# Optimization experiments

Measured on AMD Instinct MI355X. Metric: run time of the kernel, lower is better.

Reference implementation:

```python
import jax, jax.numpy as jnp
import numpy as np

N_NODES = 50000


def sage_conv(x, edge_index, W_l, b_l, W_r):
    # PyG SAGEConv (mean aggr): out_i = lin_l(mean_{j->i} x_j) + lin_r(x_i)
    src, dst = edge_index[0], edge_index[1]
    msgs = x[src]                                        # [E, C] gather
    summed = jax.ops.segment_sum(msgs, dst, num_segments=N_NODES)  # [N, C]
    deg = jax.ops.segment_sum(jnp.ones((edge_index.shape[1],), x.dtype), dst,
                              num_segments=N_NODES)
    mean = summed / jnp.maximum(deg, 1.0)[:, None]
    return mean @ W_l + b_l + x @ W_r


def setup_inputs() -> dict:
    key = jax.random.key(0)
    ks = jax.random.split(key, 12)
    E, EL, C, X = 800000, 1000000, 128, 384
    return {
        "x": jax.random.normal(ks[0], (N_NODES, X), jnp.float32),
        "edge_index": jax.random.randint(ks[1], (2, E), 0, N_NODES),
        "edge_label_index": jax.random.randint(ks[2], (2, EL), 0, N_NODES),
        "W_lin": jax.random.normal(ks[3], (X, C), jnp.float32) * 0.05,
        "b_lin": jax.random.normal(ks[4], (C,), jnp.float32) * 0.05,
        "W1_l": jax.random.normal(ks[5], (C, C), jnp.float32) * 0.08,
        "b1": jax.random.normal(ks[6], (C,), jnp.float32) * 0.05,
        "W1_r": jax.random.normal(ks[7], (C, C), jnp.float32) * 0.08,
        "W2_l": jax.random.normal(ks[8], (C, C), jnp.float32) * 0.08,
        "b2": jax.random.normal(ks[9], (C,), jnp.float32) * 0.05,
        "W2_r": jax.random.normal(ks[10], (C, C), jnp.float32) * 0.08,
    }


def reference(x, edge_index, edge_label_index, W_lin, b_lin,
              W1_l, b1, W1_r, W2_l, b2, W2_r):
    h = x @ W_lin + b_lin                                # label_lin
    h = jax.nn.relu(sage_conv(h, edge_index, W1_l, b1, W1_r))
    h = sage_conv(h, edge_index, W2_l, b2, W2_r)
    # Classifier: dot product of head/tail node features per label edge
    head = h[edge_label_index[0]]
    tail = h[edge_label_index[1]]
    return (head * tail).sum(axis=-1)                    # [EL]
```

## Files before the change

### kernel.cpp

```cpp
#include <hip/hip_runtime.h>

#define NODES 50000
#define CH 128
#define ELLW 64

using frag_ab = __attribute__((ext_vector_type(8))) short;
using frag_cd = __attribute__((ext_vector_type(4))) float;

__device__ __forceinline__ float bf2f(ushort u) {
    union { unsigned u; float f; } v; v.u = ((unsigned)u) << 16; return v.f;
}
__device__ __forceinline__ ushort f2bf(float f) {
    union { float f; unsigned u; } v; v.f = f;
    unsigned r = v.u + 0x7fff + ((v.u >> 16) & 1);
    return (ushort)(r >> 16);
}

__global__ void prep_weights(const float* __restrict__ Wlin,
                             const float* __restrict__ W1l, const float* __restrict__ W1r,
                             const float* __restrict__ W2l, const float* __restrict__ W2r,
                             ushort* __restrict__ o0, ushort* __restrict__ o1,
                             ushort* __restrict__ o2, ushort* __restrict__ o3,
                             ushort* __restrict__ o4, int* __restrict__ degs) {
    int b = blockIdx.x;
    if (b >= 448) {
        int i = (b - 448) * 256 + threadIdx.y * 128 + threadIdx.x;
        if (i < NODES) degs[i << 4] = 0;
        return;
    }
    const float* W; ushort* O; int K; int kb;
    if (b < 192) { W = Wlin; O = o0; K = 384; kb = b; }
    else {
        int j = (b - 192) >> 6; kb = (b - 192) & 63; K = 128;
        W = (j == 0) ? W1l : (j == 1) ? W1r : (j == 2) ? W2l : W2r;
        O = (j == 0) ? o1  : (j == 1) ? o2  : (j == 2) ? o3  : o4;
    }
    int k = kb * 2 + threadIdx.y;
    int n = threadIdx.x;
    if (k < K) O[(size_t)n * K + k] = f2bf(W[(size_t)k * 128 + n]);
}

__global__ __launch_bounds__(256) void lin_and_ell(
    const float* __restrict__ A, const ushort* __restrict__ Wt,
    const float* __restrict__ bias, ushort* __restrict__ out, int N, int GB,
    const int* __restrict__ ei, int E, int* __restrict__ degs, ushort* __restrict__ ell)
{
    __shared__ ushort As[128 * 32];
    __shared__ ushort Bs[128 * 32];
    if (blockIdx.x >= GB) {
        int e0 = ((blockIdx.x - GB) * 256 + threadIdx.x) * 4;
        if (e0 >= E) return;
        int s[4], dd[4], cnt;
        if (((E & 3) == 0) && (e0 + 3 < E)) {
            int4 sv = *(const int4*)(ei + e0);
            int4 dv = *(const int4*)(ei + E + e0);
            s[0] = sv.x; s[1] = sv.y; s[2] = sv.z; s[3] = sv.w;
            dd[0] = dv.x; dd[1] = dv.y; dd[2] = dv.z; dd[3] = dv.w;
            cnt = 4;
        } else {
            cnt = E - e0; if (cnt > 4) cnt = 4;
#pragma unroll
            for (int j = 0; j < 4; ++j) {
                int e = (j < cnt) ? e0 + j : e0;
                s[j] = ei[e]; dd[j] = ei[E + e];
            }
        }
#pragma unroll
        for (int j = 0; j < 4; ++j) {
            if (j < cnt) {
                int pos = atomicAdd(&degs[dd[j] << 4], 1);
                if (pos < ELLW) ell[(size_t)dd[j] * ELLW + pos] = (ushort)s[j];
            }
        }
        return;
    }
    const int tid = threadIdx.x;
    const int lane = tid & 63;
    const int wave = tid >> 6;
    const int wr = wave >> 1, wc = wave & 1;
    const int row0 = blockIdx.x * 128;
    const int l15 = lane & 15, quad = lane >> 4;

    frag_cd acc[4][4];
#pragma unroll
    for (int i = 0; i < 4; ++i)
#pragma unroll
        for (int j = 0; j < 4; ++j) acc[i][j] = (frag_cd){0.f, 0.f, 0.f, 0.f};

#pragma unroll 1
    for (int k0 = 0; k0 < 384; k0 += 32) {
        __syncthreads();
#pragma unroll
        for (int i = 0; i < 4; ++i) {
            int e = i * 256 + tid;
            int r = e >> 3, q = e & 7;
            int gr = row0 + r; if (gr > N - 1) gr = N - 1;
            float4 v = *(const float4*)(A + (size_t)gr * 384 + k0 + q * 4);
            ushort4 o; o.x = f2bf(v.x); o.y = f2bf(v.y); o.z = f2bf(v.z); o.w = f2bf(v.w);
            *(ushort4*)(As + r * 32 + q * 4) = o;
        }
#pragma unroll
        for (int i = 0; i < 2; ++i) {
            int e = i * 256 + tid;
            uint4 v = *(const uint4*)(Wt + (size_t)(e >> 2) * 384 + k0 + (e & 3) * 8);
            *(uint4*)(Bs + e * 8) = v;
        }
        __syncthreads();

        frag_ab a[4], b[4];
#pragma unroll
        for (int i = 0; i < 4; ++i)
            a[i] = *(const frag_ab*)(As + (wr * 64 + i * 16 + l15) * 32 + quad * 8);
#pragma unroll
        for (int j = 0; j < 4; ++j)
            b[j] = *(const frag_ab*)(Bs + (wc * 64 + j * 16 + l15) * 32 + quad * 8);
#pragma unroll
        for (int i = 0; i < 4; ++i)
#pragma unroll
            for (int j = 0; j < 4; ++j)
                acc[i][j] = __builtin_amdgcn_mfma_f32_16x16x32_bf16(a[i], b[j], acc[i][j], 0, 0, 0);
    }

#pragma unroll
    for (int i = 0; i < 4; ++i)
#pragma unroll
        for (int r = 0; r < 4; ++r) {
            int row = row0 + wr * 64 + i * 16 + quad * 4 + r;
            if (row < N)
#pragma unroll
                for (int j = 0; j < 4; ++j) {
                    int col = wc * 64 + j * 16 + l15;
                    out[(size_t)row * 128 + col] = f2bf(acc[i][j][r] + bias[col]);
                }
        }
}

__device__ __forceinline__ void acc8(float* acc, uint4 v) {
    acc[0] += bf2f((ushort)(v.x & 0xffff)); acc[1] += bf2f((ushort)(v.x >> 16));
    acc[2] += bf2f((ushort)(v.y & 0xffff)); acc[3] += bf2f((ushort)(v.y >> 16));
    acc[4] += bf2f((ushort)(v.z & 0xffff)); acc[5] += bf2f((ushort)(v.z >> 16));
    acc[6] += bf2f((ushort)(v.w & 0xffff)); acc[7] += bf2f((ushort)(v.w >> 16));
}

template <bool RELU>
__global__ __launch_bounds__(256) void agg_gemm(
    const ushort* __restrict__ h, const ushort* __restrict__ ell,
    const int* __restrict__ degs,
    const ushort* __restrict__ Wtl, const ushort* __restrict__ Wtr,
    const float* __restrict__ bias, ushort* __restrict__ out, int N)
{
    __shared__ ushort Ms[64 * 128];
    __shared__ ushort As[64 * 32];
    __shared__ ushort Bs[128 * 32];
    const int tid = threadIdx.x;
    const int lane = tid & 63;
    const int wave = tid >> 6;
    const int row0 = blockIdx.x * 64;
    const int g = lane >> 4;
    const int q = lane & 15;

#pragma unroll 1
    for (int it = 0; it < 4; ++it) {
        int r = (wave << 4) + (it << 2) + g;
        int node = row0 + r;
        int nd = node < N ? node : N - 1;
        const ushort* erow = ell + (size_t)nd * ELLW;
        int d = degs[nd << 4];
        int dc = d < ELLW ? d : ELLW;
        float acc[8];
#pragma unroll
        for (int k = 0; k < 8; ++k) acc[k] = 0.f;
        int n = 0;
        for (; n + 8 <= dc; n += 8) {
            ushort4 iv0 = *(const ushort4*)(erow + n);
            ushort4 iv1 = *(const ushort4*)(erow + n + 4);
            uint4 v0 = *(const uint4*)(h + (size_t)iv0.x * CH + q * 8);
            uint4 v1 = *(const uint4*)(h + (size_t)iv0.y * CH + q * 8);
            uint4 v2 = *(const uint4*)(h + (size_t)iv0.z * CH + q * 8);
            uint4 v3 = *(const uint4*)(h + (size_t)iv0.w * CH + q * 8);
            uint4 v4 = *(const uint4*)(h + (size_t)iv1.x * CH + q * 8);
            uint4 v5 = *(const uint4*)(h + (size_t)iv1.y * CH + q * 8);
            uint4 v6 = *(const uint4*)(h + (size_t)iv1.z * CH + q * 8);
            uint4 v7 = *(const uint4*)(h + (size_t)iv1.w * CH + q * 8);
            acc8(acc, v0); acc8(acc, v1); acc8(acc, v2); acc8(acc, v3);
            acc8(acc, v4); acc8(acc, v5); acc8(acc, v6); acc8(acc, v7);
        }
        for (; n + 4 <= dc; n += 4) {
            ushort4 iv = *(const ushort4*)(erow + n);
            uint4 v0 = *(const uint4*)(h + (size_t)iv.x * CH + q * 8);
            uint4 v1 = *(const uint4*)(h + (size_t)iv.y * CH + q * 8);
            uint4 v2 = *(const uint4*)(h + (size_t)iv.z * CH + q * 8);
            uint4 v3 = *(const uint4*)(h + (size_t)iv.w * CH + q * 8);
            acc8(acc, v0); acc8(acc, v1); acc8(acc, v2); acc8(acc, v3);
        }
        for (; n < dc; ++n) {
            uint4 v0 = *(const uint4*)(h + (size_t)erow[n] * CH + q * 8);
            acc8(acc, v0);
        }
        float inv = 1.f / fmaxf((float)d, 1.f);
        uint4 o;
        o.x = ((uint)f2bf(acc[1] * inv) << 16) | (uint)f2bf(acc[0] * inv);
        o.y = ((uint)f2bf(acc[3] * inv) << 16) | (uint)f2bf(acc[2] * inv);
        o.z = ((uint)f2bf(acc[5] * inv) << 16) | (uint)f2bf(acc[4] * inv);
        o.w = ((uint)f2bf(acc[7] * inv) << 16) | (uint)f2bf(acc[6] * inv);
        int chunk = q ^ (r & 7);
        *(uint4*)(Ms + r * 128 + chunk * 8) = o;
    }

    const int wr = wave >> 1, wc = wave & 1;
    const int l15 = q, quad = g;

    frag_cd acc2[2][4];
#pragma unroll
    for (int i = 0; i < 2; ++i)
#pragma unroll
        for (int j = 0; j < 4; ++j) acc2[i][j] = (frag_cd){0.f, 0.f, 0.f, 0.f};

#pragma unroll 1
    for (int part = 0; part < 2; ++part) {
        const ushort* Wt = part ? Wtr : Wtl;
#pragma unroll 1
        for (int k0 = 0; k0 < 128; k0 += 32) {
            __syncthreads();
            if (part) {
                int rr = tid >> 2, kq = tid & 3;
                int gr = row0 + rr; if (gr > N - 1) gr = N - 1;
                uint4 v = *(const uint4*)(h + (size_t)gr * CH + k0 + kq * 8);
                *(uint4*)(As + rr * 32 + ((kq ^ (rr & 3)) * 8)) = v;
            }
#pragma unroll
            for (int i2 = 0; i2 < 2; ++i2) {
                int e = i2 * 256 + tid;
                int br = e >> 2, bk = e & 3;
                uint4 v = *(const uint4*)(Wt + (size_t)br * 128 + k0 + bk * 8);
                *(uint4*)(Bs + br * 32 + ((bk ^ (br & 3)) * 8)) = v;
            }
            __syncthreads();

            frag_ab a[2], b[4];
#pragma unroll
            for (int i = 0; i < 2; ++i) {
                int ar = wr * 32 + i * 16 + l15;
                if (part) {
                    a[i] = *(const frag_ab*)(As + ar * 32 + ((quad ^ (ar & 3)) * 8));
                } else {
                    int ch = ((k0 >> 3) + quad) ^ (ar & 7);
                    a[i] = *(const frag_ab*)(Ms + ar * 128 + ch * 8);
                }
            }
#pragma unroll
            for (int j = 0; j < 4; ++j) {
                int br = wc * 64 + j * 16 + l15;
                b[j] = *(const frag_ab*)(Bs + br * 32 + ((quad ^ (br & 3)) * 8));
            }
#pragma unroll
            for (int i = 0; i < 2; ++i)
#pragma unroll
                for (int j = 0; j < 4; ++j)
                    acc2[i][j] = __builtin_amdgcn_mfma_f32_16x16x32_bf16(a[i], b[j], acc2[i][j], 0, 0, 0);
        }
    }

#pragma unroll
    for (int i = 0; i < 2; ++i)
#pragma unroll
        for (int rr = 0; rr < 4; ++rr) {
            int row = row0 + wr * 32 + i * 16 + quad * 4 + rr;
            if (row < N)
#pragma unroll
                for (int j = 0; j < 4; ++j) {
                    int col = wc * 64 + j * 16 + l15;
                    float v = acc2[i][j][rr] + bias[col];
                    if (RELU) v = fmaxf(v, 0.f);
                    out[(size_t)row * 128 + col] = f2bf(v);
                }
        }
}

__device__ __forceinline__ float dot8(uint4 va, uint4 vb) {
    float p = 0.f;
    p += bf2f((ushort)(va.x & 0xffff)) * bf2f((ushort)(vb.x & 0xffff));
    p += bf2f((ushort)(va.x >> 16))    * bf2f((ushort)(vb.x >> 16));
    p += bf2f((ushort)(va.y & 0xffff)) * bf2f((ushort)(vb.y & 0xffff));
    p += bf2f((ushort)(va.y >> 16))    * bf2f((ushort)(vb.y >> 16));
    p += bf2f((ushort)(va.z & 0xffff)) * bf2f((ushort)(vb.z & 0xffff));
    p += bf2f((ushort)(va.z >> 16))    * bf2f((ushort)(vb.z >> 16));
    p += bf2f((ushort)(va.w & 0xffff)) * bf2f((ushort)(vb.w & 0xffff));
    p += bf2f((ushort)(va.w >> 16))    * bf2f((ushort)(vb.w >> 16));
    return p;
}

__global__ __launch_bounds__(256) void classify_bf(
    const ushort* __restrict__ h2, const int* __restrict__ eli,
    int EL, float* __restrict__ out) {
    int gt = blockIdx.x * blockDim.x + threadIdx.x;
    int g0 = (gt >> 4) * 8;
    int lane = gt & 15;
    if (g0 >= EL) return;
    bool full = (g0 + 7 < EL);
    int ha[8], ta[8];
    if (full) {
        int4 h0 = *(const int4*)(eli + g0);
        int4 h1 = *(const int4*)(eli + g0 + 4);
        int4 t0 = *(const int4*)(eli + EL + g0);
        int4 t1 = *(const int4*)(eli + EL + g0 + 4);
        ha[0] = h0.x; ha[1] = h0.y; ha[2] = h0.z; ha[3] = h0.w;
        ha[4] = h1.x; ha[5] = h1.y; ha[6] = h1.z; ha[7] = h1.w;
        ta[0] = t0.x; ta[1] = t0.y; ta[2] = t0.z; ta[3] = t0.w;
        ta[4] = t1.x; ta[5] = t1.y; ta[6] = t1.z; ta[7] = t1.w;
    } else {
#pragma unroll
        for (int j = 0; j < 8; ++j) {
            int gj = (g0 + j < EL) ? g0 + j : EL - 1;
            ha[j] = eli[gj];
            ta[j] = eli[EL + gj];
        }
    }
    uint4 va[8], vb[8];
#pragma unroll
    for (int j = 0; j < 8; ++j) {
        va[j] = *((const uint4*)(h2 + (size_t)ha[j] * CH) + lane);
        vb[j] = *((const uint4*)(h2 + (size_t)ta[j] * CH) + lane);
    }
    float p[8];
#pragma unroll
    for (int j = 0; j < 8; ++j) p[j] = dot8(va[j], vb[j]);
#pragma unroll
    for (int s = 8; s >= 1; s >>= 1) {
#pragma unroll
        for (int j = 0; j < 8; ++j) p[j] += __shfl_down(p[j], s, 16);
    }
    if (lane == 0) {
        if (full) {
            *(float4*)(out + g0)     = make_float4(p[0], p[1], p[2], p[3]);
            *(float4*)(out + g0 + 4) = make_float4(p[4], p[5], p[6], p[7]);
        } else {
#pragma unroll
            for (int j = 0; j < 8; ++j)
                if (g0 + j < EL) out[g0 + j] = p[j];
        }
    }
}

extern "C" void kernel_launch(void* const* d_in, const int* in_sizes, int n_in,
                              void* d_out, int out_size, void* d_ws, size_t ws_size,
                              hipStream_t stream) {
    const float* x     = (const float*)d_in[0];
    const int*   ei    = (const int*)d_in[1];
    const int*   eli   = (const int*)d_in[2];
    const float* W_lin = (const float*)d_in[3];
    const float* b_lin = (const float*)d_in[4];
    const float* W1l   = (const float*)d_in[5];
    const float* b1    = (const float*)d_in[6];
    const float* W1r   = (const float*)d_in[7];
    const float* W2l   = (const float*)d_in[8];
    const float* b2    = (const float*)d_in[9];
    const float* W2r   = (const float*)d_in[10];
    float* out = (float*)d_out;

    const int E  = in_sizes[1] / 2;
    const int EL = in_sizes[2] / 2;
    const int N  = NODES;

    char* ws = (char*)d_ws;
    size_t off = 0;
    auto alloc = [&](size_t bytes) -> void* {
        void* p = ws + off;
        off += (bytes + 255) & ~(size_t)255;
        return p;
    };
    ushort* n0    = (ushort*)alloc((size_t)N * CH * sizeof(ushort));
    ushort* n1    = (ushort*)alloc((size_t)N * CH * sizeof(ushort));
    ushort* n2    = (ushort*)alloc((size_t)N * CH * sizeof(ushort));
    ushort* WtLin = (ushort*)alloc((size_t)CH * 384 * sizeof(ushort));
    ushort* Wt1l  = (ushort*)alloc((size_t)CH * CH * sizeof(ushort));
    ushort* Wt1r  = (ushort*)alloc((size_t)CH * CH * sizeof(ushort));
    ushort* Wt2l  = (ushort*)alloc((size_t)CH * CH * sizeof(ushort));
    ushort* Wt2r  = (ushort*)alloc((size_t)CH * CH * sizeof(ushort));
    int* degs = (int*)alloc((size_t)N * 16 * sizeof(int));
    ushort* ell = (ushort*)alloc((size_t)N * ELLW * sizeof(ushort));
    (void)ws_size; (void)n_in; (void)out_size;

    const int GB128 = (N + 127) / 128;
    const int EB4   = (E + 1023) / 1024;
    const int AB64  = (N + 63) / 64;

    prep_weights<<<dim3(644), dim3(128, 2), 0, stream>>>(
        W_lin, W1l, W1r, W2l, W2r, WtLin, Wt1l, Wt1r, Wt2l, Wt2r, degs);

    lin_and_ell<<<dim3(GB128 + EB4), dim3(256), 0, stream>>>(
        x, WtLin, b_lin, n0, N, GB128, ei, E, degs, ell);

    agg_gemm<true><<<dim3(AB64), dim3(256), 0, stream>>>(
        n0, ell, degs, Wt1l, Wt1r, b1, n2, N);

    agg_gemm<false><<<dim3(AB64), dim3(256), 0, stream>>>(
        n2, ell, degs, Wt2l, Wt2r, b2, n1, N);

    long long groups = ((long long)EL + 7) / 8;
    long long cls_threads = groups * 16;
    classify_bf<<<dim3((int)((cls_threads + 255) / 256)), dim3(256), 0, stream>>>(
        n1, eli, EL, out);
}
```

Baseline: 299.4 us.

## Build ELL adjacency with range-partitioned LDS atomics instead of global atomics

Each of 64 blocks owns a contiguous range of destination nodes, scans the full dst array, and counts and places edges using shared-memory atomics. Degrees are then written compactly, which removes the padded degree array and its zeroing in the weight-prep kernel. This avoids contended global atomics but makes every partition block re-read the whole edge list, which may become the critical path.

```diff
diff --git a/kernel.cpp b/kernel.cpp
--- a/kernel.cpp
+++ b/kernel.cpp
@@ -3,6 +3,7 @@
 #define NODES 50000
 #define CH 128
 #define ELLW 64
+#define RBLK 64
 
 using frag_ab = __attribute__((ext_vector_type(8))) short;
 using frag_cd = __attribute__((ext_vector_type(4))) float;
@@ -21,13 +22,8 @@
                              const float* __restrict__ W2l, const float* __restrict__ W2r,
                              ushort* __restrict__ o0, ushort* __restrict__ o1,
                              ushort* __restrict__ o2, ushort* __restrict__ o3,
-                             ushort* __restrict__ o4, int* __restrict__ degs) {
+                             ushort* __restrict__ o4) {
     int b = blockIdx.x;
-    if (b >= 448) {
-        int i = (b - 448) * 256 + threadIdx.y * 128 + threadIdx.x;
-        if (i < NODES) degs[i << 4] = 0;
-        return;
-    }
     const float* W; ushort* O; int K; int kb;
     if (b < 192) { W = Wlin; O = o0; K = 384; kb = b; }
     else {
@@ -42,43 +38,62 @@
 
 __global__ __launch_bounds__(256) void lin_and_ell(
     const float* __restrict__ A, const ushort* __restrict__ Wt,
-    const float* __restrict__ bias, ushort* __restrict__ out, int N, int GB,
+    const float* __restrict__ bias, ushort* __restrict__ out, int N,
     const int* __restrict__ ei, int E, int* __restrict__ degs, ushort* __restrict__ ell)
 {
     __shared__ ushort As[128 * 32];
     __shared__ ushort Bs[128 * 32];
-    if (blockIdx.x >= GB) {
-        int e0 = ((blockIdx.x - GB) * 256 + threadIdx.x) * 4;
-        if (e0 >= E) return;
-        int s[4], dd[4], cnt;
-        if (((E & 3) == 0) && (e0 + 3 < E)) {
-            int4 sv = *(const int4*)(ei + e0);
-            int4 dv = *(const int4*)(ei + E + e0);
-            s[0] = sv.x; s[1] = sv.y; s[2] = sv.z; s[3] = sv.w;
-            dd[0] = dv.x; dd[1] = dv.y; dd[2] = dv.z; dd[3] = dv.w;
-            cnt = 4;
+    __shared__ int cnt[800];
+
+    if (blockIdx.x < RBLK) {
+        const int RNG = (N + RBLK - 1) / RBLK;
+        const int lo = blockIdx.x * RNG;
+        const int hi = (lo + RNG < N) ? lo + RNG : N;
+        const int nr = hi - lo;
+        for (int i = threadIdx.x; i < nr; i += 256) cnt[i] = 0;
+        __syncthreads();
+
+        const int* dst = ei + E;
+        if ((E & 3) == 0) {
+            const int E4 = E >> 2;
+            int c = threadIdx.x;
+            for (; c + 256 < E4; c += 512) {
+                int4 da = *(const int4*)(dst + (size_t)c * 4);
+                int4 db = *(const int4*)(dst + (size_t)(c + 256) * 4);
+                int ea = c * 4, eb = (c + 256) * 4;
+                if (da.x >= lo && da.x < hi) { int p = atomicAdd(&cnt[da.x - lo], 1); if (p < ELLW) ell[(size_t)da.x * ELLW + p] = (ushort)ei[ea];     }
+                if (da.y >= lo && da.y < hi) { int p = atomicAdd(&cnt[da.y - lo], 1); if (p < ELLW) ell[(size_t)da.y * ELLW + p] = (ushort)ei[ea + 1]; }
+                if (da.z >= lo && da.z < hi) { int p = atomicAdd(&cnt[da.z - lo], 1); if (p < ELLW) ell[(size_t)da.z * ELLW + p] = (ushort)ei[ea + 2]; }
+                if (da.w >= lo && da.w < hi) { int p = atomicAdd(&cnt[da.w - lo], 1); if (p < ELLW) ell[(size_t)da.w * ELLW + p] = (ushort)ei[ea + 3]; }
+                if (db.x >= lo && db.x < hi) { int p = atomicAdd(&cnt[db.x - lo], 1); if (p < ELLW) ell[(size_t)db.x * ELLW + p] = (ushort)ei[eb];     }
+                if (db.y >= lo && db.y < hi) { int p = atomicAdd(&cnt[db.y - lo], 1); if (p < ELLW) ell[(size_t)db.y * ELLW + p] = (ushort)ei[eb + 1]; }
+                if (db.z >= lo && db.z < hi) { int p = atomicAdd(&cnt[db.z - lo], 1); if (p < ELLW) ell[(size_t)db.z * ELLW + p] = (ushort)ei[eb + 2]; }
+                if (db.w >= lo && db.w < hi) { int p = atomicAdd(&cnt[db.w - lo], 1); if (p < ELLW) ell[(size_t)db.w * ELLW + p] = (ushort)ei[eb + 3]; }
+            }
+            for (; c < E4; c += 256) {
+                int4 da = *(const int4*)(dst + (size_t)c * 4);
+                int ea = c * 4;
+                if (da.x >= lo && da.x < hi) { int p = atomicAdd(&cnt[da.x - lo], 1); if (p < ELLW) ell[(size_t)da.x * ELLW + p] = (ushort)ei[ea];     }
+                if (da.y >= lo && da.y < hi) { int p = atomicAdd(&cnt[da.y - lo], 1); if (p < ELLW) ell[(size_t)da.y * ELLW + p] = (ushort)ei[ea + 1]; }
+                if (da.z >= lo && da.z < hi) { int p = atomicAdd(&cnt[da.z - lo], 1); if (p < ELLW) ell[(size_t)da.z * ELLW + p] = (ushort)ei[ea + 2]; }
+                if (da.w >= lo && da.w < hi) { int p = atomicAdd(&cnt[da.w - lo], 1); if (p < ELLW) ell[(size_t)da.w * ELLW + p] = (ushort)ei[ea + 3]; }
+            }
         } else {
-            cnt = E - e0; if (cnt > 4) cnt = 4;
-#pragma unroll
-            for (int j = 0; j < 4; ++j) {
-                int e = (j < cnt) ? e0 + j : e0;
-                s[j] = ei[e]; dd[j] = ei[E + e];
-            }
-        }
-#pragma unroll
-        for (int j = 0; j < 4; ++j) {
-            if (j < cnt) {
-                int pos = atomicAdd(&degs[dd[j] << 4], 1);
-                if (pos < ELLW) ell[(size_t)dd[j] * ELLW + pos] = (ushort)s[j];
-            }
-        }
+            for (int e = threadIdx.x; e < E; e += 256) {
+                int d = dst[e];
+                if (d >= lo && d < hi) { int p = atomicAdd(&cnt[d - lo], 1); if (p < ELLW) ell[(size_t)d * ELLW + p] = (ushort)ei[e]; }
+            }
+        }
+        __syncthreads();
+        for (int i = threadIdx.x; i < nr; i += 256) degs[lo + i] = cnt[i];
         return;
     }
+
     const int tid = threadIdx.x;
     const int lane = tid & 63;
     const int wave = tid >> 6;
     const int wr = wave >> 1, wc = wave & 1;
-    const int row0 = blockIdx.x * 128;
+    const int row0 = (blockIdx.x - RBLK) * 128;
     const int l15 = lane & 15, quad = lane >> 4;
 
     frag_cd acc[4][4];
@@ -165,7 +180,7 @@
         int node = row0 + r;
         int nd = node < N ? node : N - 1;
         const ushort* erow = ell + (size_t)nd * ELLW;
-        int d = degs[nd << 4];
+        int d = degs[nd];
         int dc = d < ELLW ? d : ELLW;
         float acc[8];
 #pragma unroll
@@ -377,19 +392,18 @@
     ushort* Wt1r  = (ushort*)alloc((size_t)CH * CH * sizeof(ushort));
     ushort* Wt2l  = (ushort*)alloc((size_t)CH * CH * sizeof(ushort));
     ushort* Wt2r  = (ushort*)alloc((size_t)CH * CH * sizeof(ushort));
-    int* degs = (int*)alloc((size_t)N * 16 * sizeof(int));
+    int* degs = (int*)alloc((size_t)N * sizeof(int));
     ushort* ell = (ushort*)alloc((size_t)N * ELLW * sizeof(ushort));
     (void)ws_size; (void)n_in; (void)out_size;
 
     const int GB128 = (N + 127) / 128;
-    const int EB4   = (E + 1023) / 1024;
     const int AB64  = (N + 63) / 64;
 
-    prep_weights<<<dim3(644), dim3(128, 2), 0, stream>>>(
-        W_lin, W1l, W1r, W2l, W2r, WtLin, Wt1l, Wt1r, Wt2l, Wt2r, degs);
-
-    lin_and_ell<<<dim3(GB128 + EB4), dim3(256), 0, stream>>>(
-        x, WtLin, b_lin, n0, N, GB128, ei, E, degs, ell);
+    prep_weights<<<dim3(448), dim3(128, 2), 0, stream>>>(
+        W_lin, W1l, W1r, W2l, W2r, WtLin, Wt1l, Wt1r, Wt2l, Wt2r);
+
+    lin_and_ell<<<dim3(RBLK + GB128), dim3(256), 0, stream>>>(
+        x, WtLin, b_lin, n0, N, ei, E, degs, ell);
 
     agg_gemm<true><<<dim3(AB64), dim3(256), 0, stream>>>(
         n0, ell, degs, Wt1l, Wt1r, b1, n2, N);
```

Result: slower. 917.4 us (+206.4%).

## Fuse pipeline into a persistent cooperative mega-kernel with grid syncs

Applied to the files above, without the earlier changes.

Turns the five separate launches (weight prep, linear+ELL fill, two aggregation GEMMs, classifier) into device-side role functions. A single cooperative persistent kernel runs them, with grid.sync between phases, and the old multi-launch path stays as a fallback. The degree array loses its 16-int padding and is cleared with a memset instead of in the prep kernel. The classifier now handles 4 label edges per 16-lane group instead of 8. The aim is to remove launch gaps and tail effects between stages. The costs are grid-wide barrier overhead, register pressure from launch_bounds(256,5), and more atomic contention on densely packed degree counters.

```diff
diff --git a/kernel.cpp b/kernel.cpp
--- a/kernel.cpp
+++ b/kernel.cpp
@@ -1,4 +1,7 @@
 #include <hip/hip_runtime.h>
+#include <hip/hip_cooperative_groups.h>
+
+namespace cg = cooperative_groups;
 
 #define NODES 50000
 #define CH 128
@@ -16,18 +19,14 @@
     return (ushort)(r >> 16);
 }
 
-__global__ void prep_weights(const float* __restrict__ Wlin,
-                             const float* __restrict__ W1l, const float* __restrict__ W1r,
-                             const float* __restrict__ W2l, const float* __restrict__ W2r,
-                             ushort* __restrict__ o0, ushort* __restrict__ o1,
-                             ushort* __restrict__ o2, ushort* __restrict__ o3,
-                             ushort* __restrict__ o4, int* __restrict__ degs) {
-    int b = blockIdx.x;
-    if (b >= 448) {
-        int i = (b - 448) * 256 + threadIdx.y * 128 + threadIdx.x;
-        if (i < NODES) degs[i << 4] = 0;
-        return;
-    }
+
+__device__ __forceinline__ void prep_role(int b, int tid,
+    const float* __restrict__ Wlin, const float* __restrict__ W1l,
+    const float* __restrict__ W1r, const float* __restrict__ W2l,
+    const float* __restrict__ W2r,
+    ushort* __restrict__ o0, ushort* __restrict__ o1, ushort* __restrict__ o2,
+    ushort* __restrict__ o3, ushort* __restrict__ o4)
+{
     const float* W; ushort* O; int K; int kb;
     if (b < 192) { W = Wlin; O = o0; K = 384; kb = b; }
     else {
@@ -35,50 +34,50 @@
         W = (j == 0) ? W1l : (j == 1) ? W1r : (j == 2) ? W2l : W2r;
         O = (j == 0) ? o1  : (j == 1) ? o2  : (j == 2) ? o3  : o4;
     }
-    int k = kb * 2 + threadIdx.y;
-    int n = threadIdx.x;
+    int k = kb * 2 + (tid >> 7);
+    int n = tid & 127;
     if (k < K) O[(size_t)n * K + k] = f2bf(W[(size_t)k * 128 + n]);
 }
 
-__global__ __launch_bounds__(256) void lin_and_ell(
+__device__ __forceinline__ void fill_role(int fb, int tid,
+    const int* __restrict__ ei, int E, int* __restrict__ degs, ushort* __restrict__ ell)
+{
+    int e0 = (fb * 256 + tid) * 4;
+    if (e0 >= E) return;
+    int s[4], dd[4], cnt;
+    if (((E & 3) == 0) && (e0 + 3 < E)) {
+        int4 sv = *(const int4*)(ei + e0);
+        int4 dv = *(const int4*)(ei + E + e0);
+        s[0] = sv.x; s[1] = sv.y; s[2] = sv.z; s[3] = sv.w;
+        dd[0] = dv.x; dd[1] = dv.y; dd[2] = dv.z; dd[3] = dv.w;
+        cnt = 4;
+    } else {
+        cnt = E - e0; if (cnt > 4) cnt = 4;
+#pragma unroll
+        for (int j = 0; j < 4; ++j) {
+            int e = (j < cnt) ? e0 + j : e0;
+            s[j] = ei[e]; dd[j] = ei[E + e];
+        }
+    }
+#pragma unroll
+    for (int j = 0; j < 4; ++j) {
+        if (j < cnt) {
+            int pos = atomicAdd(&degs[dd[j]], 1);
+            if (pos < ELLW) ell[(size_t)dd[j] * ELLW + pos] = (ushort)s[j];
+        }
+    }
+}
+
+__device__ __forceinline__ void lin_gemm_role(int gb, int tid, ushort* smem,
     const float* __restrict__ A, const ushort* __restrict__ Wt,
-    const float* __restrict__ bias, ushort* __restrict__ out, int N, int GB,
-    const int* __restrict__ ei, int E, int* __restrict__ degs, ushort* __restrict__ ell)
-{
-    __shared__ ushort As[128 * 32];
-    __shared__ ushort Bs[128 * 32];
-    if (blockIdx.x >= GB) {
-        int e0 = ((blockIdx.x - GB) * 256 + threadIdx.x) * 4;
-        if (e0 >= E) return;
-        int s[4], dd[4], cnt;
-        if (((E & 3) == 0) && (e0 + 3 < E)) {
-            int4 sv = *(const int4*)(ei + e0);
-            int4 dv = *(const int4*)(ei + E + e0);
-            s[0] = sv.x; s[1] = sv.y; s[2] = sv.z; s[3] = sv.w;
-            dd[0] = dv.x; dd[1] = dv.y; dd[2] = dv.z; dd[3] = dv.w;
-            cnt = 4;
-        } else {
-            cnt = E - e0; if (cnt > 4) cnt = 4;
-#pragma unroll
-            for (int j = 0; j < 4; ++j) {
-                int e = (j < cnt) ? e0 + j : e0;
-                s[j] = ei[e]; dd[j] = ei[E + e];
-            }
-        }
-#pragma unroll
-        for (int j = 0; j < 4; ++j) {
-            if (j < cnt) {
-                int pos = atomicAdd(&degs[dd[j] << 4], 1);
-                if (pos < ELLW) ell[(size_t)dd[j] * ELLW + pos] = (ushort)s[j];
-            }
-        }
-        return;
-    }
-    const int tid = threadIdx.x;
+    const float* __restrict__ bias, ushort* __restrict__ out, int N)
+{
+    ushort* As = smem;
+    ushort* Bs = smem + 4096;
     const int lane = tid & 63;
     const int wave = tid >> 6;
     const int wr = wave >> 1, wc = wave & 1;
-    const int row0 = blockIdx.x * 128;
+    const int row0 = gb * 128;
     const int l15 = lane & 15, quad = lane >> 4;
 
     frag_cd acc[4][4];
@@ -142,20 +141,18 @@
     acc[6] += bf2f((ushort)(v.w & 0xffff)); acc[7] += bf2f((ushort)(v.w >> 16));
 }
 
-template <bool RELU>
-__global__ __launch_bounds__(256) void agg_gemm(
+__device__ __forceinline__ void agg_role(int ab, int tid, ushort* smem,
     const ushort* __restrict__ h, const ushort* __restrict__ ell,
     const int* __restrict__ degs,
     const ushort* __restrict__ Wtl, const ushort* __restrict__ Wtr,
-    const float* __restrict__ bias, ushort* __restrict__ out, int N)
-{
-    __shared__ ushort Ms[64 * 128];
-    __shared__ ushort As[64 * 32];
-    __shared__ ushort Bs[128 * 32];
-    const int tid = threadIdx.x;
+    const float* __restrict__ bias, ushort* __restrict__ out, int N, bool relu)
+{
+    ushort* Ms = smem;
+    ushort* As = smem + 8192;
+    ushort* Bs = smem + 10240;
     const int lane = tid & 63;
     const int wave = tid >> 6;
-    const int row0 = blockIdx.x * 64;
+    const int row0 = ab * 64;
     const int g = lane >> 4;
     const int q = lane & 15;
 
@@ -165,7 +162,7 @@
         int node = row0 + r;
         int nd = node < N ? node : N - 1;
         const ushort* erow = ell + (size_t)nd * ELLW;
-        int d = degs[nd << 4];
+        int d = degs[nd];
         int dc = d < ELLW ? d : ELLW;
         float acc[8];
 #pragma unroll
@@ -271,7 +268,7 @@
                 for (int j = 0; j < 4; ++j) {
                     int col = wc * 64 + j * 16 + l15;
                     float v = acc2[i][j][rr] + bias[col];
-                    if (RELU) v = fmaxf(v, 0.f);
+                    if (relu) v = fmaxf(v, 0.f);
                     out[(size_t)row * 128 + col] = f2bf(v);
                 }
         }
@@ -290,56 +287,130 @@
     return p;
 }
 
-__global__ __launch_bounds__(256) void classify_bf(
-    const ushort* __restrict__ h2, const int* __restrict__ eli,
-    int EL, float* __restrict__ out) {
-    int gt = blockIdx.x * blockDim.x + threadIdx.x;
-    int g0 = (gt >> 4) * 8;
+__device__ __forceinline__ void classify_role(int cb, int tid,
+    const ushort* __restrict__ h2, const int* __restrict__ eli, int EL,
+    float* __restrict__ out)
+{
+    int gt = cb * 256 + tid;
+    int g0 = (gt >> 4) * 4;
     int lane = gt & 15;
     if (g0 >= EL) return;
-    bool full = (g0 + 7 < EL);
-    int ha[8], ta[8];
+    bool full = (g0 + 3 < EL);
+    int ha[4], ta[4];
     if (full) {
-        int4 h0 = *(const int4*)(eli + g0);
-        int4 h1 = *(const int4*)(eli + g0 + 4);
-        int4 t0 = *(const int4*)(eli + EL + g0);
-        int4 t1 = *(const int4*)(eli + EL + g0 + 4);
-        ha[0] = h0.x; ha[1] = h0.y; ha[2] = h0.z; ha[3] = h0.w;
-        ha[4] = h1.x; ha[5] = h1.y; ha[6] = h1.z; ha[7] = h1.w;
-        ta[0] = t0.x; ta[1] = t0.y; ta[2] = t0.z; ta[3] = t0.w;
-        ta[4] = t1.x; ta[5] = t1.y; ta[6] = t1.z; ta[7] = t1.w;
+        int4 hv = *(const int4*)(eli + g0);
+        int4 tv = *(const int4*)(eli + EL + g0);
+        ha[0] = hv.x; ha[1] = hv.y; ha[2] = hv.z; ha[3] = hv.w;
+        ta[0] = tv.x; ta[1] = tv.y; ta[2] = tv.z; ta[3] = tv.w;
     } else {
 #pragma unroll
-        for (int j = 0; j < 8; ++j) {
+        for (int j = 0; j < 4; ++j) {
             int gj = (g0 + j < EL) ? g0 + j : EL - 1;
             ha[j] = eli[gj];
             ta[j] = eli[EL + gj];
         }
     }
-    uint4 va[8], vb[8];
-#pragma unroll
-    for (int j = 0; j < 8; ++j) {
+    uint4 va[4], vb[4];
+#pragma unroll
+    for (int j = 0; j < 4; ++j) {
         va[j] = *((const uint4*)(h2 + (size_t)ha[j] * CH) + lane);
         vb[j] = *((const uint4*)(h2 + (size_t)ta[j] * CH) + lane);
     }
-    float p[8];
-#pragma unroll
-    for (int j = 0; j < 8; ++j) p[j] = dot8(va[j], vb[j]);
+    float p[4];
+#pragma unroll
+    for (int j = 0; j < 4; ++j) p[j] = dot8(va[j], vb[j]);
 #pragma unroll
     for (int s = 8; s >= 1; s >>= 1) {
 #pragma unroll
-        for (int j = 0; j < 8; ++j) p[j] += __shfl_down(p[j], s, 16);
+        for (int j = 0; j < 4; ++j) p[j] += __shfl_down(p[j], s, 16);
     }
     if (lane == 0) {
         if (full) {
-            *(float4*)(out + g0)     = make_float4(p[0], p[1], p[2], p[3]);
-            *(float4*)(out + g0 + 4) = make_float4(p[4], p[5], p[6], p[7]);
+            *(float4*)(out + g0) = make_float4(p[0], p[1], p[2], p[3]);
         } else {
 #pragma unroll
-            for (int j = 0; j < 8; ++j)
+            for (int j = 0; j < 4; ++j)
                 if (g0 + j < EL) out[g0 + j] = p[j];
         }
     }
+}
+
+__global__ __launch_bounds__(256, 5) void mega(
+    const float* __restrict__ x, const int* __restrict__ ei, const int* __restrict__ eli,
+    const float* __restrict__ Wlin, const float* __restrict__ blin,
+    const float* __restrict__ W1l, const float* __restrict__ b1, const float* __restrict__ W1r,
+    const float* __restrict__ W2l, const float* __restrict__ b2, const float* __restrict__ W2r,
+    float* __restrict__ out,
+    ushort* __restrict__ n0, ushort* __restrict__ n1, ushort* __restrict__ n2,
+    ushort* __restrict__ WtLin, ushort* __restrict__ Wt1l, ushort* __restrict__ Wt1r,
+    ushort* __restrict__ Wt2l, ushort* __restrict__ Wt2r,
+    int* __restrict__ degs, ushort* __restrict__ ell, int E, int EL)
+{
+    __shared__ ushort smem[14336];
+    cg::grid_group grid = cg::this_grid();
+    const int bid = blockIdx.x;
+    const int tid = threadIdx.x;
+    const int GSZ = gridDim.x;
+    const int N  = NODES;
+    const int EB = (E + 1023) / 1024;
+    const int GB = (N + 127) / 128;
+    const int AB = (N + 63) / 64;
+    const int CB = (EL + 63) / 64;
+
+    for (int vb = bid; vb < 448; vb += GSZ)
+        prep_role(vb, tid, Wlin, W1l, W1r, W2l, W2r, WtLin, Wt1l, Wt1r, Wt2l, Wt2r);
+    grid.sync();
+
+    for (int vb = bid; vb < EB + GB; vb += GSZ) {
+        if (vb < EB) fill_role(vb, tid, ei, E, degs, ell);
+        else         lin_gemm_role(vb - EB, tid, smem, x, WtLin, blin, n0, N);
+    }
+    grid.sync();
+
+    for (int vb = bid; vb < AB; vb += GSZ)
+        agg_role(vb, tid, smem, n0, ell, degs, Wt1l, Wt1r, b1, n2, N, true);
+    grid.sync();
+
+    for (int vb = bid; vb < AB; vb += GSZ)
+        agg_role(vb, tid, smem, n2, ell, degs, Wt2l, Wt2r, b2, n1, N, false);
+    grid.sync();
+
+    for (int cb = bid; cb < CB; cb += GSZ)
+        classify_role(cb, tid, n1, eli, EL, out);
+}
+
+__global__ __launch_bounds__(256) void k_prep(
+    const float* Wlin, const float* W1l, const float* W1r,
+    const float* W2l, const float* W2r,
+    ushort* o0, ushort* o1, ushort* o2, ushort* o3, ushort* o4)
+{
+    if (blockIdx.x < 448)
+        prep_role(blockIdx.x, threadIdx.x, Wlin, W1l, W1r, W2l, W2r, o0, o1, o2, o3, o4);
+}
+
+__global__ __launch_bounds__(256) void k_linfill(
+    const float* A, const ushort* Wt, const float* bias, ushort* out, int N,
+    const int* ei, int E, int* degs, ushort* ell)
+{
+    __shared__ ushort smem[8192];
+    int EB = (E + 1023) / 1024;
+    int b = blockIdx.x;
+    if (b < EB) fill_role(b, threadIdx.x, ei, E, degs, ell);
+    else        lin_gemm_role(b - EB, threadIdx.x, smem, A, Wt, bias, out, N);
+}
+
+__global__ __launch_bounds__(256) void k_agg(
+    const ushort* h, const ushort* ell, const int* degs,
+    const ushort* Wtl, const ushort* Wtr, const float* bias, ushort* out, int N, int relu)
+{
+    __shared__ ushort smem[14336];
+    agg_role(blockIdx.x, threadIdx.x, smem, h, ell, degs, Wtl, Wtr, bias, out, N, relu != 0);
+}
+
+__global__ __launch_bounds__(256) void k_cls(
+    const ushort* h2, const int* eli, int EL, float* out)
+{
+    classify_role(blockIdx.x, threadIdx.x, h2, eli, EL, out);
 }
 
 extern "C" void kernel_launch(void* const* d_in, const int* in_sizes, int n_in,
@@ -358,9 +429,9 @@
     const float* W2r   = (const float*)d_in[10];
     float* out = (float*)d_out;
 
-    const int E  = in_sizes[1] / 2;
-    const int EL = in_sizes[2] / 2;
-    const int N  = NODES;
+    int E  = in_sizes[1] / 2;
+    int EL = in_sizes[2] / 2;
+    const int N = NODES;
 
     char* ws = (char*)d_ws;
     size_t off = 0;
@@ -377,28 +448,48 @@
     ushort* Wt1r  = (ushort*)alloc((size_t)CH * CH * sizeof(ushort));
     ushort* Wt2l  = (ushort*)alloc((size_t)CH * CH * sizeof(ushort));
     ushort* Wt2r  = (ushort*)alloc((size_t)CH * CH * sizeof(ushort));
-    int* degs = (int*)alloc((size_t)N * 16 * sizeof(int));
+    int* degs = (int*)alloc((size_t)N * sizeof(int));
     ushort* ell = (ushort*)alloc((size_t)N * ELLW * sizeof(ushort));
     (void)ws_size; (void)n_in; (void)out_size;
 
-    const int GB128 = (N + 127) / 128;
-    const int EB4   = (E + 1023) / 1024;
-    const int AB64  = (N + 63) / 64;
-
-    prep_weights<<<dim3(644), dim3(128, 2), 0, stream>>>(
-        W_lin, W1l, W1r, W2l, W2r, WtLin, Wt1l, Wt1r, Wt2l, Wt2r, degs);
-
-    lin_and_ell<<<dim3(GB128 + EB4), dim3(256), 0, stream>>>(
-        x, WtLin, b_lin, n0, N, GB128, ei, E, degs, ell);
-
-    agg_gemm<true><<<dim3(AB64), dim3(256), 0, stream>>>(
-        n0, ell, degs, Wt1l, Wt1r, b1, n2, N);
-
-    agg_gemm<false><<<dim3(AB64), dim3(256), 0, stream>>>(
-        n2, ell, degs, Wt2l, Wt2r, b2, n1, N);
-
-    long long groups = ((long long)EL + 7) / 8;
-    long long cls_threads = groups * 16;
-    classify_bf<<<dim3((int)((cls_threads + 255) / 256)), dim3(256), 0, stream>>>(
-        n1, eli, EL, out);
-}
+    const int EB = (E + 1023) / 1024;
+    const int GB = (N + 127) / 128;
+    const int AB = (N + 63) / 64;
+    const int CB = (EL + 63) / 64;
+
+    hipMemsetAsync(degs, 0, (size_t)N * sizeof(int), stream);
+
+    static int s_grid = 0;
+    if (s_grid == 0) {
+        int occ = 0, ncu = 0, dev = 0;
+        if (hipOccupancyMaxActiveBlocksPerMultiprocessor(&occ, (const void*)mega, 256, 0) == hipSuccess &&
+            hipGetDevice(&dev) == hipSuccess) {
+            hipDeviceProp_t prop;
+            if (hipGetDeviceProperties(&prop, dev) == hipSuccess) ncu = prop.multiProcessorCount;
+        }
+        s_grid = (occ > 0 && ncu > 0) ? occ * ncu : -1;
+    }
+
+    bool coop_done = false;
+    if (s_grid >= EB + GB) {
+        int grid = s_grid;
+        void* args[] = { &x, &ei, &eli, &W_lin, &b_lin, &W1l, &b1, &W1r, &W2l, &b2, &W2r,
+                         &out, &n0, &n1, &n2, &WtLin, &Wt1l, &Wt1r, &Wt2l, &Wt2r,
+                         &degs, &ell, &E, &EL };
+        if (hipLaunchCooperativeKernel((const void*)mega, dim3(grid), dim3(256),
+                                       args, 0, stream) == hipSuccess)
+            coop_done = true;
+    }
+
+    if (!coop_done) {
+        k_prep<<<dim3(448), dim3(256), 0, stream>>>(
+            W_lin, W1l, W1r, W2l, W2r, WtLin, Wt1l, Wt1r, Wt2l, Wt2r);
+        k_linfill<<<dim3(EB + GB), dim3(256), 0, stream>>>(
+            x, WtLin, b_lin, n0, N, ei, E, degs, ell);
+        k_agg<<<dim3(AB), dim3(256), 0, stream>>>(
+            n0, ell, degs, Wt1l, Wt1r, b1, n2, N, 1);
+        k_agg<<<dim3(AB), dim3(256), 0, stream>>>(
+            n2, ell, degs, Wt2l, Wt2r, b2, n1, N, 0);
+        k_cls<<<dim3(CB), dim3(256), 0, stream>>>(n1, eli, EL, out);
+    }
+}
```

Result: slower. 338.8 us (+13.1%).

## Partition ELL build by destination range per XCD and compact degree array

Applied to the files above, without the earlier changes.

Edge blocks now take a chunk of edges and process only destinations falling in one of eight node ranges, picked by block index modulo 8, so each XCD's atomics hit a disjoint node slice. The degree counter array is compacted from 64-byte-strided to dense ints. The aim is to cut cross-die atomic traffic and cache-line waste, at the cost of each edge being read eight times.

```diff
diff --git a/kernel.cpp b/kernel.cpp
--- a/kernel.cpp
+++ b/kernel.cpp
@@ -25,7 +25,7 @@
     int b = blockIdx.x;
     if (b >= 448) {
         int i = (b - 448) * 256 + threadIdx.y * 128 + threadIdx.x;
-        if (i < NODES) degs[i << 4] = 0;
+        if (i < NODES) degs[i] = 0;
         return;
     }
     const float* W; ushort* O; int K; int kb;
@@ -48,28 +48,31 @@
     __shared__ ushort As[128 * 32];
     __shared__ ushort Bs[128 * 32];
     if (blockIdx.x >= GB) {
-        int e0 = ((blockIdx.x - GB) * 256 + threadIdx.x) * 4;
-        if (e0 >= E) return;
-        int s[4], dd[4], cnt;
-        if (((E & 3) == 0) && (e0 + 3 < E)) {
-            int4 sv = *(const int4*)(ei + e0);
-            int4 dv = *(const int4*)(ei + E + e0);
-            s[0] = sv.x; s[1] = sv.y; s[2] = sv.z; s[3] = sv.w;
-            dd[0] = dv.x; dd[1] = dv.y; dd[2] = dv.z; dd[3] = dv.w;
-            cnt = 4;
+        const int fb = blockIdx.x - GB;
+        const int rr = blockIdx.x & 7;
+        const int chunk = fb >> 3;
+        const int RNG = (NODES + 7) / 8;
+        const int lo = rr * RNG;
+        int hi = lo + RNG; if (hi > N) hi = N;
+        const int ce = (((E + 97) / 98) + 3) & ~3;
+        const int start = chunk * ce;
+        int end = start + ce; if (end > E) end = E;
+        if (start >= E) return;
+        const int* srcp = ei;
+        const int* dstp = ei + E;
+        if ((E & 3) == 0) {
+            for (int e = start + threadIdx.x * 4; e < end; e += 1024) {
+                int4 dv = *(const int4*)(dstp + e);
+                int4 sv = *(const int4*)(srcp + e);
+                if (dv.x >= lo && dv.x < hi) { int p = atomicAdd(&degs[dv.x], 1); if (p < ELLW) ell[(size_t)dv.x * ELLW + p] = (ushort)sv.x; }
+                if (dv.y >= lo && dv.y < hi) { int p = atomicAdd(&degs[dv.y], 1); if (p < ELLW) ell[(size_t)dv.y * ELLW + p] = (ushort)sv.y; }
+                if (dv.z >= lo && dv.z < hi) { int p = atomicAdd(&degs[dv.z], 1); if (p < ELLW) ell[(size_t)dv.z * ELLW + p] = (ushort)sv.z; }
+                if (dv.w >= lo && dv.w < hi) { int p = atomicAdd(&degs[dv.w], 1); if (p < ELLW) ell[(size_t)dv.w * ELLW + p] = (ushort)sv.w; }
+            }
         } else {
-            cnt = E - e0; if (cnt > 4) cnt = 4;
-#pragma unroll
-            for (int j = 0; j < 4; ++j) {
-                int e = (j < cnt) ? e0 + j : e0;
-                s[j] = ei[e]; dd[j] = ei[E + e];
-            }
-        }
-#pragma unroll
-        for (int j = 0; j < 4; ++j) {
-            if (j < cnt) {
-                int pos = atomicAdd(&degs[dd[j] << 4], 1);
-                if (pos < ELLW) ell[(size_t)dd[j] * ELLW + pos] = (ushort)s[j];
+            for (int e = start + threadIdx.x; e < end; e += 256) {
+                int d = dstp[e];
+                if (d >= lo && d < hi) { int p = atomicAdd(&degs[d], 1); if (p < ELLW) ell[(size_t)d * ELLW + p] = (ushort)srcp[e]; }
             }
         }
         return;
@@ -165,7 +168,7 @@
         int node = row0 + r;
         int nd = node < N ? node : N - 1;
         const ushort* erow = ell + (size_t)nd * ELLW;
-        int d = degs[nd << 4];
+        int d = degs[nd];
         int dc = d < ELLW ? d : ELLW;
         float acc[8];
 #pragma unroll
@@ -377,18 +380,20 @@
     ushort* Wt1r  = (ushort*)alloc((size_t)CH * CH * sizeof(ushort));
     ushort* Wt2l  = (ushort*)alloc((size_t)CH * CH * sizeof(ushort));
     ushort* Wt2r  = (ushort*)alloc((size_t)CH * CH * sizeof(ushort));
-    int* degs = (int*)alloc((size_t)N * 16 * sizeof(int));
+    int* degs = (int*)alloc((size_t)N * sizeof(int));
     ushort* ell = (ushort*)alloc((size_t)N * ELLW * sizeof(ushort));
     (void)ws_size; (void)n_in; (void)out_size;
 
     const int GB128 = (N + 127) / 128;
-    const int EB4   = (E + 1023) / 1024;
-    const int AB64  = (N + 63) / 64;
+    const int ce     = (((E + 97) / 98) + 3) & ~3;
+    const int chunks = (E + ce - 1) / ce;
+    const int FB     = chunks * 8;
+    const int AB64   = (N + 63) / 64;
 
     prep_weights<<<dim3(644), dim3(128, 2), 0, stream>>>(
         W_lin, W1l, W1r, W2l, W2r, WtLin, Wt1l, Wt1r, Wt2l, Wt2r, degs);
 
-    lin_and_ell<<<dim3(GB128 + EB4), dim3(256), 0, stream>>>(
+    lin_and_ell<<<dim3(GB128 + FB), dim3(256), 0, stream>>>(
         x, WtLin, b_lin, n0, N, GB128, ei, E, degs, ell);
 
     agg_gemm<true><<<dim3(AB64), dim3(256), 0, stream>>>(
```

New measurement: 310.2 us. 3.6% more time.
